# Kernel optimization log

Hardware: AMD Instinct MI355X
Metric: run time of the kernel (lower is better)

## Reference

```python
import jax, jax.numpy as jnp
import numpy as np

D_MODEL = 5120
NUM_HEADS = 128
HEAD_DIM = D_MODEL // NUM_HEADS  # 40
LATENT = 1536


def setup_inputs() -> dict:
    key = jax.random.key(0)
    ks = jax.random.split(key, 9)
    B, S = 2, 1024
    scale = 0.02
    return {
        "x": jax.random.normal(ks[0], (B, S, D_MODEL), dtype=jnp.float32),
        "Wq": jax.random.normal(ks[1], (D_MODEL, D_MODEL), dtype=jnp.float32) * scale,
        "bq": jnp.zeros((D_MODEL,), dtype=jnp.float32),
        "Wc": jax.random.normal(ks[2], (D_MODEL, LATENT), dtype=jnp.float32) * scale,
        "bc": jnp.zeros((LATENT,), dtype=jnp.float32),
        "Wk": jax.random.normal(ks[3], (LATENT, D_MODEL), dtype=jnp.float32) * scale,
        "bk": jnp.zeros((D_MODEL,), dtype=jnp.float32),
        "Wv": jax.random.normal(ks[4], (LATENT, D_MODEL), dtype=jnp.float32) * scale,
        "bv": jnp.zeros((D_MODEL,), dtype=jnp.float32),
    }


def reference(x, Wq, bq, Wc, bc, Wk, bk, Wv, bv):
    B, S, _ = x.shape
    H, Dh = NUM_HEADS, HEAD_DIM
    # projections
    q = x @ Wq + bq                     # [B,S,D]
    kv_latent = x @ Wc + bc             # [B,S,L]
    k = kv_latent @ Wk + bk             # [B,S,D]
    v = kv_latent @ Wv + bv             # [B,S,D]
    # split heads -> [B,H,S,Dh]
    q = q.reshape(B, S, H, Dh).transpose(0, 2, 1, 3)
    k = k.reshape(B, S, H, Dh).transpose(0, 2, 1, 3)
    v = v.reshape(B, S, H, Dh).transpose(0, 2, 1, 3)
    scores = jnp.einsum("bhqd,bhkd->bhqk", q, k) / jnp.sqrt(jnp.float32(Dh))
    attn = jax.nn.softmax(scores, axis=-1)
    out = jnp.einsum("bhqk,bhkd->bhqd", attn, v)  # [B,H,S,Dh]
    return out.transpose(0, 2, 1, 3).reshape(B, S, H * Dh)
```

## Files before the change

### kernel.cpp

```cpp
#include <hip/hip_runtime.h>
#include <hip/hip_bf16.h>

typedef __attribute__((ext_vector_type(8))) __bf16 bf16x8;
typedef __attribute__((ext_vector_type(4))) __bf16 bf16x4;
typedef __attribute__((ext_vector_type(4))) float f32x4;

#define MFMA16(a, b, c) __builtin_amdgcn_mfma_f32_16x16x32_bf16((a), (b), (c), 0, 0, 0)

#if __has_builtin(__builtin_amdgcn_exp2f)
#define EXP2F(x) __builtin_amdgcn_exp2f(x)
#else
#define EXP2F(x) exp2f(x)
#endif

#define GLDS16(g, l)                                                             \
    __builtin_amdgcn_global_load_lds((const __attribute__((address_space(1))) void*)(g), \
                                     (__attribute__((address_space(3))) void*)(l), 16, 0, 0)

#define BARRIER()                          \
    do {                                   \
        asm volatile("" ::: "memory");     \
        __builtin_amdgcn_s_barrier();      \
        asm volatile("" ::: "memory");     \
    } while (0)

#define WAIT_LGKM0() asm volatile("s_waitcnt lgkmcnt(0)" ::: "memory")
#define VM6 asm volatile("s_waitcnt vmcnt(6)" ::: "memory")
#define VM0 asm volatile("s_waitcnt vmcnt(0)" ::: "memory")
#define VMNONE ((void)0)
#define KEEP(x) x
#define DROP(x)

static __device__ __forceinline__ unsigned short cvt_bf(float f) {
    return __builtin_bit_cast(unsigned short, (__bf16)f);
}

static __device__ __forceinline__ bf16x8 bf8_zero() {
    uint4 z = make_uint4(0, 0, 0, 0);
    return __builtin_bit_cast(bf16x8, z);
}

__global__ __launch_bounds__(256) void xconv(const float* __restrict__ X,
                                             unsigned short* __restrict__ Xb, int n) {
    int i = (blockIdx.x * 256 + threadIdx.x) * 4;
    if (i < n) {
        float4 f = *(const float4*)(X + i);
        ushort4 o;
        o.x = cvt_bf(f.x); o.y = cvt_bf(f.y); o.z = cvt_bf(f.z); o.w = cvt_bf(f.w);
        *(ushort4*)(Xb + i) = o;
    }
}

__global__ __launch_bounds__(256) void wconv(const float* __restrict__ W,
                                             unsigned short* __restrict__ WT, int K, int N) {
    __shared__ unsigned short tile[32][33];
    int n0 = blockIdx.x * 32, k0 = blockIdx.y * 32;
    int c = threadIdx.x & 31, r8 = threadIdx.x >> 5;
#pragma unroll
    for (int it = 0; it < 4; ++it) {
        int r = r8 + it * 8;
        tile[r][c] = cvt_bf(W[(size_t)(k0 + r) * N + n0 + c]);
    }
    __syncthreads();
    int k2 = (threadIdx.x & 15) * 2, n8 = threadIdx.x >> 4;
#pragma unroll
    for (int it = 0; it < 2; ++it) {
        int n = n8 + it * 16;
        ushort2 o;
        o.x = tile[k2][n];
        o.y = tile[k2 + 1][n];
        *(ushort2*)&WT[(size_t)(n0 + n) * K + k0 + k2] = o;
    }
}


#define STAGE_A(S, H, KT)                                                              \
    do {                                                                               \
        GLDS16(aS[H][0] + (size_t)(KT) * 64, &Abuf[S][(H) * 8192 + wid * 512]);        \
        GLDS16(aS[H][1] + (size_t)(KT) * 64, &Abuf[S][(H) * 8192 + 4096 + wid * 512]); \
    } while (0)
#define STAGE_B(S, H, KT)                                                              \
    do {                                                                               \
        GLDS16(bS[H][0] + (size_t)(KT) * 64, &Bbuf[S][(H) * 8192 + wid * 512]);        \
        GLDS16(bS[H][1] + (size_t)(KT) * 64, &Bbuf[S][(H) * 8192 + 4096 + wid * 512]); \
    } while (0)

#define LDA_HALF(S, QM)                                                                   \
    do {                                                                                  \
        _Pragma("unroll") for (int mi = 0; mi < 4; ++mi)                                  \
            _Pragma("unroll") for (int kh = 0; kh < 2; ++kh)                              \
                af[mi][kh] =                                                              \
                    *(const bf16x8*)&Abuf[S][((QM) * 8192 + aoff + mi * 1024) ^ (kh * 32)]; \
    } while (0)
#define LDB_HALF(S, QN, BF)                                                               \
    do {                                                                                  \
        _Pragma("unroll") for (int ni = 0; ni < 2; ++ni)                                  \
            _Pragma("unroll") for (int kh = 0; kh < 2; ++kh)                              \
                BF[ni][kh] =                                                              \
                    *(const bf16x8*)&Bbuf[S][((QN) * 8192 + boff + ni * 1024) ^ (kh * 32)]; \
    } while (0)

#define MMAQ(QM, QN, BF)                                                                \
    do {                                                                                \
        _Pragma("unroll") for (int mi = 0; mi < 4; ++mi)                                \
            _Pragma("unroll") for (int ni = 0; ni < 2; ++ni)                            \
                _Pragma("unroll") for (int kh = 0; kh < 2; ++kh)                        \
                    acc[(QM) * 4 + mi][(QN) * 2 + ni] =                                 \
                        MFMA16(af[mi][kh], BF[ni][kh], acc[(QM) * 4 + mi][(QN) * 2 + ni]); \
    } while (0)

#define KTILE(S, T, STG1, STG234, VMOP)             \
    {                                               \
        const int s_ = (S);                         \
        LDA_HALF(s_, 0);                            \
        LDB_HALF(s_, 0, bf0);                       \
        STG1(STAGE_B(s_ ^ 1, 0, (T) + 1);)          \
        asm volatile("s_waitcnt lgkmcnt(8)" ::: "memory"); \
        BARRIER();                                  \
        WAIT_LGKM0();                               \
        __builtin_amdgcn_s_setprio(1);              \
        MMAQ(0, 0, bf0);                            \
        __builtin_amdgcn_s_setprio(0);              \
        BARRIER();                                  \
        LDB_HALF(s_, 1, bf1);                       \
        STG234(STAGE_A(s_, 0, (T) + 2);)            \
        BARRIER();                                  \
        WAIT_LGKM0();                               \
        __builtin_amdgcn_s_setprio(1);              \
        MMAQ(0, 1, bf1);                            \
        __builtin_amdgcn_s_setprio(0);              \
        BARRIER();                                  \
        LDA_HALF(s_, 1);                            \
        STG234(STAGE_B(s_, 1, (T) + 2);)            \
        BARRIER();                                  \
        WAIT_LGKM0();                               \
        __builtin_amdgcn_s_setprio(1);              \
        MMAQ(1, 1, bf1);                            \
        __builtin_amdgcn_s_setprio(0);              \
        BARRIER();                                  \
        STG234(STAGE_A(s_, 1, (T) + 2);)            \
        VMOP;                                       \
        BARRIER();                                  \
        __builtin_amdgcn_s_setprio(1);              \
        MMAQ(1, 0, bf0);                            \
        __builtin_amdgcn_s_setprio(0);              \
        BARRIER();                                  \
    }

__global__ __launch_bounds__(512, 2) void gemm256(const unsigned short* __restrict__ A, int lda,
                                                  const unsigned short* __restrict__ BT, int ldb,
                                                  const float* __restrict__ bias0,
                                                  const float* __restrict__ bias1, int nsplit,
                                                  unsigned short* __restrict__ C, int ldc,
                                                  int K, float s0, float s1, int gx) {
    __shared__ __align__(16) unsigned short Abuf[2][16384];
    __shared__ __align__(16) unsigned short Bbuf[2][16384];

    int nwg = gridDim.x, orig = blockIdx.x;
    int cpx = nwg >> 3;
    int wgid = (orig & 7) * cpx + (orig >> 3);
    int tm = wgid / gx, tn = wgid % gx;
    int m0 = tm * 256, n0 = tn * 256;

    int tid = threadIdx.x, lane = tid & 63, wid = tid >> 6;
    int wm = wid >> 2, wn = wid & 3;
    int lrow = lane & 15, lkg = lane >> 4;

    int t5 = tid >> 3;
    int cole = ((tid & 7) ^ ((tid >> 3) & 7)) << 3;
    const unsigned short* aS[2][2];
    const unsigned short* bS[2][2];
#pragma unroll
    for (int H = 0; H < 2; ++H)
#pragma unroll
        for (int c = 0; c < 2; ++c) {
            int rA = (c << 7) | (H << 6) | t5;
            int rB = (((c << 1) | (t5 >> 5)) << 6) | (H << 5) | (t5 & 31);
            aS[H][c] = A + (size_t)(m0 + rA) * lda + cole;
            bS[H][c] = BT + (size_t)(n0 + rB) * ldb + cole;
        }

    int xorc = (lkg * 8) ^ ((lrow & 7) << 3);
    int aoff = wm * 4096 + lrow * 64 + xorc;
    int boff = wn * 2048 + lrow * 64 + xorc;

    f32x4 acc[8][4];
#pragma unroll
    for (int i = 0; i < 8; ++i)
#pragma unroll
        for (int j = 0; j < 4; ++j) acc[i][j] = (f32x4){0.f, 0.f, 0.f, 0.f};
    bf16x8 af[4][2], bf0[2][2], bf1[2][2];

    const int nkt = K >> 6;

    STAGE_A(0, 0, 0); STAGE_A(0, 1, 0); STAGE_B(0, 0, 0); STAGE_B(0, 1, 0);
    STAGE_A(1, 0, 1); STAGE_B(1, 1, 1); STAGE_A(1, 1, 1);
    VM6;
    BARRIER();

    int t = 0;
    for (; t + 2 < nkt; ++t) KTILE(t & 1, t, KEEP, KEEP, VM6);
    KTILE(t & 1, t, KEEP, DROP, VM0);
    ++t;
    KTILE(t & 1, t, DROP, DROP, VMNONE);

#pragma unroll
    for (int ni = 0; ni < 4; ++ni) {
        int col = n0 + wn * 64 + ni * 16 + lrow;
        float bval = (col < nsplit) ? bias0[col] : bias1[col - nsplit];
        float scl = (col < nsplit) ? s0 : s1;
#pragma unroll
        for (int mi = 0; mi < 8; ++mi) {
            int row = m0 + wm * 128 + mi * 16 + lkg * 4;
#pragma unroll
            for (int j = 0; j < 4; ++j)
                C[(size_t)(row + j) * ldc + col] = cvt_bf((acc[mi][ni][j] + bval) * scl);
        }
    }
}

__global__ __launch_bounds__(256) void attn(const unsigned short* __restrict__ q, int ldq,
                                            const unsigned short* __restrict__ k, int ldk,
                                            const unsigned short* __restrict__ v, int ldv,
                                            float* __restrict__ out) {
    const int S = 1024, D = 5120, Dh = 40;
    int b = blockIdx.z, h = blockIdx.y, qt = blockIdx.x;
    int t = threadIdx.x, lane = t & 63, wid = t >> 6;
    int lrow = lane & 15, lkg = lane >> 4;

    __shared__ __align__(16) unsigned short Ks[64 * 72];
    __shared__ __align__(16) unsigned short Vs[64 * 72];
    __shared__ __align__(16) unsigned short Ps[4][16 * 72];

    const size_t qbase = ((size_t)b * S) * ldq + (size_t)h * Dh;
    const size_t kbase = ((size_t)b * S) * ldk + (size_t)h * Dh;
    const size_t vbase = ((size_t)b * S) * ldv + (size_t)h * Dh;
    int q0 = qt * 64 + wid * 16;

    bf16x8 qf0, qf1;
    {
        const unsigned short* qp = q + qbase + (size_t)(q0 + lrow) * ldq;
        qf0 = *(const bf16x8*)(qp + lkg * 8);
        qf1 = (lkg == 0) ? *(const bf16x8*)(qp + 32) : bf8_zero();
    }

    f32x4 acc[3];
#pragma unroll
    for (int nb = 0; nb < 3; ++nb) acc[nb] = (f32x4){0.f, 0.f, 0.f, 0.f};
    float mrun = -INFINITY, lrun = 0.f;

    for (int kt = 0; kt < 16; ++kt) {
        __syncthreads();
#pragma unroll
        for (int it = 0; it < 2; ++it) {
            int idx = t + it * 256;
            int rr = idx >> 3, cc = idx & 7;
            uint4 val = make_uint4(0, 0, 0, 0);
            if (cc < 5) val = *(const uint4*)(k + kbase + (size_t)(kt * 64 + rr) * ldk + cc * 8);
            *(uint4*)&Ks[rr * 72 + cc * 8] = val;
        }
#pragma unroll
        for (int it = 0; it < 2; ++it) {
            int idx = t + it * 256;
            int rr = idx & 63, cc = idx >> 6;
            if (cc < 6) {
                uint4 val = make_uint4(0, 0, 0, 0);
                if (cc < 5) val = *(const uint4*)(v + vbase + (size_t)(kt * 64 + rr) * ldv + cc * 8);
                const unsigned short* pv = (const unsigned short*)&val;
#pragma unroll
                for (int j = 0; j < 8; ++j) Vs[(cc * 8 + j) * 72 + rr] = pv[j];
            }
        }
        __syncthreads();

        f32x4 sf[4];
#pragma unroll
        for (int nb = 0; nb < 4; ++nb) {
            sf[nb] = (f32x4){0.f, 0.f, 0.f, 0.f};
            bf16x8 kf0 = *(const bf16x8*)&Ks[(nb * 16 + lrow) * 72 + lkg * 8];
            bf16x8 kf1 = *(const bf16x8*)&Ks[(nb * 16 + lrow) * 72 + 32 + lkg * 8];
            sf[nb] = MFMA16(kf0, qf0, sf[nb]);
            sf[nb] = MFMA16(kf1, qf1, sf[nb]);
        }

        float tm = sf[0][0];
#pragma unroll
        for (int nb = 0; nb < 4; ++nb)
#pragma unroll
            for (int i = 0; i < 4; ++i) tm = fmaxf(tm, sf[nb][i]);
        tm = fmaxf(tm, __shfl_xor(tm, 16));
        tm = fmaxf(tm, __shfl_xor(tm, 32));
        float mn = fmaxf(mrun, tm);
        float al = EXP2F(mrun - mn);
        mrun = mn;
        float rs = 0.f;
#pragma unroll
        for (int nb = 0; nb < 4; ++nb) {
            bf16x4 pk;
#pragma unroll
            for (int i = 0; i < 4; ++i) {
                float p = EXP2F(sf[nb][i] - mn);
                rs += p;
                pk[i] = (__bf16)p;
            }
            *(bf16x4*)&Ps[wid][lrow * 72 + nb * 16 + lkg * 4] = pk;
        }
        rs += __shfl_xor(rs, 16);
        rs += __shfl_xor(rs, 32);
        lrun = lrun * al + rs;

        float alr[4];
#pragma unroll
        for (int i = 0; i < 4; ++i) alr[i] = __shfl(al, lkg * 4 + i);
#pragma unroll
        for (int nb = 0; nb < 3; ++nb)
#pragma unroll
            for (int i = 0; i < 4; ++i) acc[nb][i] *= alr[i];

#pragma unroll
        for (int kk = 0; kk < 2; ++kk) {
            bf16x8 pf = *(const bf16x8*)&Ps[wid][lrow * 72 + kk * 32 + lkg * 8];
#pragma unroll
            for (int nb = 0; nb < 3; ++nb) {
                bf16x8 vf = *(const bf16x8*)&Vs[(nb * 16 + lrow) * 72 + kk * 32 + lkg * 8];
                acc[nb] = MFMA16(pf, vf, acc[nb]);
            }
        }
    }

    float lr[4];
#pragma unroll
    for (int i = 0; i < 4; ++i) lr[i] = __shfl(lrun, lkg * 4 + i);
#pragma unroll
    for (int i = 0; i < 4; ++i) {
        float inv = 1.0f / lr[i];
        int s = q0 + lkg * 4 + i;
#pragma unroll
        for (int nb = 0; nb < 3; ++nb) {
            int d = nb * 16 + lrow;
            if (d < Dh) out[((size_t)(b * S + s)) * D + h * Dh + d] = acc[nb][i] * inv;
        }
    }
}

extern "C" void kernel_launch(void* const* d_in, const int* in_sizes, int n_in,
                              void* d_out, int out_size, void* d_ws, size_t ws_size,
                              hipStream_t stream) {
    const int M = 2048, D = 5120, L = 1536, NQ = D + L , NKV = 2 * D ;
    const float* x  = (const float*)d_in[0];
    const float* Wq = (const float*)d_in[1];
    const float* bq = (const float*)d_in[2];
    const float* Wc = (const float*)d_in[3];
    const float* bc = (const float*)d_in[4];
    const float* Wk = (const float*)d_in[5];
    const float* bk = (const float*)d_in[6];
    const float* Wv = (const float*)d_in[7];
    const float* bv = (const float*)d_in[8];
    float* out = (float*)d_out;

    unsigned short* ws = (unsigned short*)d_ws;
    size_t off = 0;
    unsigned short* xb    = ws + off; off += (size_t)M * D;
    unsigned short* WqcT  = ws + off; off += (size_t)NQ * D;
    unsigned short* WkvT  = ws + off; off += (size_t)NKV * L;
    unsigned short* qkvb  = ws + off; off += (size_t)M * NQ;
    unsigned short* kvout = ws + off; off += (size_t)M * NKV;

    xconv<<<(M * D) / 1024, 256, 0, stream>>>(x, xb, M * D);
    wconv<<<dim3(D / 32, D / 32), 256, 0, stream>>>(Wq, WqcT, D, D);
    wconv<<<dim3(L / 32, D / 32), 256, 0, stream>>>(Wc, WqcT + (size_t)D * D, D, L);
    wconv<<<dim3(D / 32, L / 32), 256, 0, stream>>>(Wk, WkvT, L, D);
    wconv<<<dim3(D / 32, L / 32), 256, 0, stream>>>(Wv, WkvT + (size_t)D * L, L, D);

    const float qscale = 1.4426950408889634f / 6.324555320336759f;

    gemm256<<<dim3((NQ / 256) * (M / 256)), 512, 0, stream>>>(xb, D, WqcT, D, bq, bc, D,
                                                              qkvb, NQ, D, qscale, 1.0f,
                                                              NQ / 256);
    gemm256<<<dim3((NKV / 256) * (M / 256)), 512, 0, stream>>>(qkvb + D, NQ, WkvT, L, bk, bv, D,
                                                               kvout, NKV, L, 1.0f, 1.0f,
                                                               NKV / 256);

    attn<<<dim3(1024 / 64, 128, 2), 256, 0, stream>>>(qkvb, NQ, kvout, NKV, kvout + D, NKV, out);
}
```

Before: 538.0 us.

## Add 128x128-tile GEMM kernel for the latent-to-KV projection

Adds a new gemm128 kernel with 128x128 output tiles, 256 threads, double-buffered LDS staging through global_load_lds with an XOR swizzle, and launch bounds allowing two blocks per CU. The K/V projection (K=1536, N=10240, M=2048) now uses it in place of the 256x256 gemm256, giving 1280 blocks instead of 320. The goal is better CU occupancy and load balance on this short-K GEMM, at the cost of less data reuse per tile and a simpler pipeline than gemm256.

Measured after the change: 511.4 us. 1.05x faster.

```diff
diff --git a/kernel.cpp b/kernel.cpp
--- a/kernel.cpp
+++ b/kernel.cpp
@@ -26,6 +26,7 @@
 
 #define WAIT_LGKM0() asm volatile("s_waitcnt lgkmcnt(0)" ::: "memory")
 #define VM6 asm volatile("s_waitcnt vmcnt(6)" ::: "memory")
+#define VM8 asm volatile("s_waitcnt vmcnt(8)" ::: "memory")
 #define VM0 asm volatile("s_waitcnt vmcnt(0)" ::: "memory")
 #define VMNONE ((void)0)
 #define KEEP(x) x
@@ -73,7 +74,6 @@
     }
 }
 
-
 #define STAGE_A(S, H, KT)                                                              \
     do {                                                                               \
         GLDS16(aS[H][0] + (size_t)(KT) * 64, &Abuf[S][(H) * 8192 + wid * 512]);        \
@@ -212,6 +212,96 @@
 #pragma unroll
         for (int mi = 0; mi < 8; ++mi) {
             int row = m0 + wm * 128 + mi * 16 + lkg * 4;
+#pragma unroll
+            for (int j = 0; j < 4; ++j)
+                C[(size_t)(row + j) * ldc + col] = cvt_bf((acc[mi][ni][j] + bval) * scl);
+        }
+    }
+}
+
+#define STG128(S, KT)                                                                  \
+    do {                                                                               \
+        _Pragma("unroll") for (int i_ = 0; i_ < 4; ++i_)                               \
+            GLDS16(Ag + (size_t)(i_ * 32) * lda + (size_t)(KT) * 64,                   \
+                   &Abuf[S][i_ * 2048 + wid * 512]);                                   \
+        _Pragma("unroll") for (int i_ = 0; i_ < 4; ++i_)                               \
+            GLDS16(Bg + (size_t)(i_ * 32) * ldb + (size_t)(KT) * 64,                   \
+                   &Bbuf[S][i_ * 2048 + wid * 512]);                                   \
+    } while (0)
+
+__global__ __launch_bounds__(256, 2) void gemm128(const unsigned short* __restrict__ A, int lda,
+                                                  const unsigned short* __restrict__ BT, int ldb,
+                                                  const float* __restrict__ bias0,
+                                                  const float* __restrict__ bias1, int nsplit,
+                                                  unsigned short* __restrict__ C, int ldc,
+                                                  int K, float s0, float s1, int gy) {
+    __shared__ __align__(16) unsigned short Abuf[2][8192];
+    __shared__ __align__(16) unsigned short Bbuf[2][8192];
+
+    int b = blockIdx.x;
+    int tm = b % gy, tn = b / gy;
+    int m0 = tm * 128, n0 = tn * 128;
+    int tid = threadIdx.x, lane = tid & 63, wid = tid >> 6;
+    int wm = wid >> 1, wn = wid & 1;
+    int lrow = lane & 15, lkg = lane >> 4;
+
+    int srow = tid >> 3;
+    int cole = ((tid & 7) ^ ((tid >> 3) & 7)) << 3;
+    const unsigned short* Ag = A + (size_t)(m0 + srow) * lda + cole;
+    const unsigned short* Bg = BT + (size_t)(n0 + srow) * ldb + cole;
+
+    int xorc8 = (lrow & 7) << 3;
+    int aoff = (wm * 64 + lrow) * 64;
+    int boff = (wn * 64 + lrow) * 64;
+
+    f32x4 acc[4][4];
+#pragma unroll
+    for (int i = 0; i < 4; ++i)
+#pragma unroll
+        for (int j = 0; j < 4; ++j) acc[i][j] = (f32x4){0.f, 0.f, 0.f, 0.f};
+
+    const int nkt = K >> 6;
+    STG128(0, 0);
+    for (int t = 0; t < nkt; ++t) {
+        const int cur = t & 1;
+        if (t + 1 < nkt) {
+            STG128(cur ^ 1, t + 1);
+            VM8;
+        } else {
+            VM0;
+        }
+        BARRIER();
+        bf16x8 af[4][2], bv[4][2];
+#pragma unroll
+        for (int mi = 0; mi < 4; ++mi)
+#pragma unroll
+            for (int kh = 0; kh < 2; ++kh)
+                af[mi][kh] = *(const bf16x8*)&Abuf[cur][aoff + mi * 1024 + (((kh * 4 + lkg) << 3) ^ xorc8)];
+#pragma unroll
+        for (int ni = 0; ni < 4; ++ni)
+#pragma unroll
+            for (int kh = 0; kh < 2; ++kh)
+                bv[ni][kh] = *(const bf16x8*)&Bbuf[cur][boff + ni * 1024 + (((kh * 4 + lkg) << 3) ^ xorc8)];
+        __builtin_amdgcn_s_setprio(1);
+#pragma unroll
+        for (int mi = 0; mi < 4; ++mi)
+#pragma unroll
+            for (int ni = 0; ni < 4; ++ni)
+#pragma unroll
+                for (int kh = 0; kh < 2; ++kh)
+                    acc[mi][ni] = MFMA16(af[mi][kh], bv[ni][kh], acc[mi][ni]);
+        __builtin_amdgcn_s_setprio(0);
+        BARRIER();
+    }
+
+#pragma unroll
+    for (int ni = 0; ni < 4; ++ni) {
+        int col = n0 + wn * 64 + ni * 16 + lrow;
+        float bval = (col < nsplit) ? bias0[col] : bias1[col - nsplit];
+        float scl = (col < nsplit) ? s0 : s1;
+#pragma unroll
+        for (int mi = 0; mi < 4; ++mi) {
+            int row = m0 + wm * 64 + mi * 16 + lkg * 4;
 #pragma unroll
             for (int j = 0; j < 4; ++j)
                 C[(size_t)(row + j) * ldc + col] = cvt_bf((acc[mi][ni][j] + bval) * scl);
@@ -377,9 +467,9 @@
     gemm256<<<dim3((NQ / 256) * (M / 256)), 512, 0, stream>>>(xb, D, WqcT, D, bq, bc, D,
                                                               qkvb, NQ, D, qscale, 1.0f,
                                                               NQ / 256);
-    gemm256<<<dim3((NKV / 256) * (M / 256)), 512, 0, stream>>>(qkvb + D, NQ, WkvT, L, bk, bv, D,
+    gemm128<<<dim3((NKV / 128) * (M / 128)), 256, 0, stream>>>(qkvb + D, NQ, WkvT, L, bk, bv, D,
                                                                kvout, NKV, L, 1.0f, 1.0f,
-                                                               NKV / 256);
+                                                               M / 128);
 
     attn<<<dim3(1024 / 64, 128, 2), 256, 0, stream>>>(qkvb, NQ, kvout, NKV, kvout + D, NKV, out);
 }
```
